# Kernel tuning notes

Measured on AMD Instinct MI355X. Metric: run time of the kernel, lower is better.

Reference implementation:

```python
import jax, jax.numpy as jnp
import numpy as np

N = 50000
E = 1000000
WIDTH = 64
DEPTH = 4


def setup_inputs() -> dict:
    key = jax.random.key(0)
    ks = jax.random.split(key, 6)
    x = jax.random.normal(ks[0], (N, 5), dtype=jnp.float32)
    edge_index = jax.random.randint(ks[1], (2, E), 0, N, dtype=jnp.int32)
    edge_attr = jax.random.normal(ks[2], (E, 3), dtype=jnp.float32)
    w1 = jax.random.normal(ks[3], (3, WIDTH), dtype=jnp.float32) / jnp.sqrt(3.0)
    b1 = jnp.zeros((WIDTH,), jnp.float32)
    w2 = jax.random.normal(ks[4], (WIDTH, 1), dtype=jnp.float32) / jnp.sqrt(float(WIDTH))
    b2 = jnp.zeros((1,), jnp.float32)
    root = jax.random.normal(ks[5], (1, 1), dtype=jnp.float32)
    bias = jnp.zeros((1,), jnp.float32)
    return dict(x=x, edge_index=edge_index, edge_attr=edge_attr,
                w1=w1, b1=b1, w2=w2, b2=b2, root=root, bias=bias)


def reference(x, edge_index, edge_attr, w1, b1, w2, b2, root, bias):
    # h: scalar node feature, column 2 of data.x -> [N, 1]
    h = x[:, 2:3]
    src, dst = edge_index[0], edge_index[1]  # messages flow src -> dst

    # Per-edge 1x1 weight from the edge MLP (depends only on edge_attr,
    # identical for all depth iterations since the conv is shared).
    w_e = jax.nn.relu(edge_attr @ w1 + b1) @ w2 + b2  # [E, 1]

    # Mean aggregation: precompute in-degree of each target node.
    deg = jax.ops.segment_sum(jnp.ones((E,), jnp.float32), dst, num_segments=N)
    inv_deg = jnp.where(deg > 0, 1.0 / jnp.maximum(deg, 1.0), 0.0)[:, None]  # [N, 1]

    for _ in range(DEPTH):
        msg = h[src] * w_e                                        # gather + per-edge weight, [E, 1]
        agg = jax.ops.segment_sum(msg, dst, num_segments=N) * inv_deg  # scatter-mean, [N, 1]
        h = jax.nn.relu(agg + h @ root + bias)                    # root transform + bias + ReLU
    return h
```

## Files before the change

### kernel.cpp

```cpp
#include <hip/hip_runtime.h>

#define NN 50000
#define NE 1000000
#define NBK 196
#define EPB 1024
#define PB 977
#define ESTRIDE 5632
#define RK 12

__global__ void init_fixed(const float* __restrict__ x, float* __restrict__ h,
                           int* __restrict__ cursor, int* __restrict__ sBeg,
                           int* __restrict__ sLim) {
    int i = blockIdx.x * 256 + threadIdx.x;
    if (i < NN) h[i] = x[5 * i + 2];
    if (i < NBK) {
        cursor[i] = i * ESTRIDE;
        sBeg[i]   = i * ESTRIDE;
        sLim[i]   = (i + 1) * ESTRIDE;
    }
}

__global__ void bucket_count(const int* __restrict__ dst, int* __restrict__ bcnt,
                             const float* __restrict__ x, float* __restrict__ h) {
    __shared__ int hist[NBK];
    int t = threadIdx.x;
    if (t < NBK) hist[t] = 0;
    __syncthreads();
    int gid = blockIdx.x * 256 + t;
    if (gid < NN) h[gid] = x[5 * gid + 2];
#pragma unroll
    for (int j = 0; j < 4; ++j) {
        int e = blockIdx.x * EPB + j * 256 + t;
        if (e < NE) atomicAdd(&hist[dst[e] >> 8], 1);
    }
    __syncthreads();
    if (t < NBK && hist[t]) atomicAdd(&bcnt[t], hist[t]);
}

__global__ void bucket_scan(const int* __restrict__ bcnt,
                            int* __restrict__ sBeg,
                            int* __restrict__ cursor,
                            int* __restrict__ sLim) {
    __shared__ int part[256];
    int t = threadIdx.x;
    int v = (t < NBK) ? ((bcnt[t] + 1) & ~1) : 0;
    part[t] = v;
    __syncthreads();
    for (int off = 1; off < 256; off <<= 1) {
        int x = part[t];
        int add = (t >= off) ? part[t - off] : 0;
        __syncthreads();
        part[t] = x + add;
        __syncthreads();
    }
    if (t < NBK) {
        int excl = part[t] - v;
        sBeg[t] = excl;
        cursor[t] = excl;
        sLim[t] = 0x7FFFFFFF;
    }
}

__global__ void place_kernel(const float* __restrict__ ea,
                             const int* __restrict__ src,
                             const int* __restrict__ dst,
                             const float* __restrict__ w1,
                             const float* __restrict__ b1,
                             const float* __restrict__ w2,
                             const float* __restrict__ b2,
                             const int* __restrict__ sLim,
                             int* __restrict__ cursor,
                             uint2* __restrict__ es,
                             int dumpbase) {
    __shared__ float sw1[192];
    __shared__ float sb1[64];
    __shared__ float sw2[64];
    __shared__ float sce[EPB];
    __shared__ int hist[NBK];
    __shared__ int hbase[NBK];
    int t = threadIdx.x;
    if (t < 192) sw1[t] = w1[t];
    if (t < 64) { sb1[t] = b1[t]; sw2[t] = w2[t]; }
    if (t < NBK) hist[t] = 0;
    __syncthreads();

    int r[4], dd[4];
#pragma unroll
    for (int j = 0; j < 4; ++j) {
        int e = blockIdx.x * EPB + j * 256 + t;
        dd[j] = -1;
        if (e < NE) {
            float a0 = ea[3 * e + 0];
            float a1 = ea[3 * e + 1];
            float a2 = ea[3 * e + 2];
            float c0 = b2[0], c1 = 0.f, c2 = 0.f, c3 = 0.f;
#pragma unroll
            for (int k = 0; k < 64; k += 4) {
                float h0 = fmaf(a0, sw1[k+0], fmaf(a1, sw1[64+k+0], fmaf(a2, sw1[128+k+0], sb1[k+0])));
                float h1 = fmaf(a0, sw1[k+1], fmaf(a1, sw1[64+k+1], fmaf(a2, sw1[128+k+1], sb1[k+1])));
                float h2 = fmaf(a0, sw1[k+2], fmaf(a1, sw1[64+k+2], fmaf(a2, sw1[128+k+2], sb1[k+2])));
                float h3 = fmaf(a0, sw1[k+3], fmaf(a1, sw1[64+k+3], fmaf(a2, sw1[128+k+3], sb1[k+3])));
                c0 = fmaf(fmaxf(h0, 0.f), sw2[k+0], c0);
                c1 = fmaf(fmaxf(h1, 0.f), sw2[k+1], c1);
                c2 = fmaf(fmaxf(h2, 0.f), sw2[k+2], c2);
                c3 = fmaf(fmaxf(h3, 0.f), sw2[k+3], c3);
            }
            sce[j * 256 + t] = (c0 + c1) + (c2 + c3);
            int d = dst[e];
            dd[j] = d;
            r[j] = atomicAdd(&hist[d >> 8], 1);
        }
    }
    __syncthreads();
    if (t < NBK) { int hv = hist[t]; if (hv) hbase[t] = atomicAdd(&cursor[t], hv); }
    __syncthreads();
#pragma unroll
    for (int j = 0; j < 4; ++j) {
        int e = blockIdx.x * EPB + j * 256 + t;
        if (e < NE) {
            int d = dd[j];
            int b = d >> 8;
            int pos = hbase[b] + r[j];
            if (pos >= sLim[b]) pos = dumpbase + (t & 63);
            unsigned pack = (unsigned)src[e] | ((unsigned)(d & 255) << 17);
            es[pos] = make_uint2(pack, __float_as_uint(sce[j * 256 + t]));
        }
    }
}

__global__ void round1_slice(const int* __restrict__ sBeg,
                             const int* __restrict__ sEnd,
                             const int* __restrict__ sLim,
                             const uint2* __restrict__ es,
                             const float* __restrict__ hold,
                             float* __restrict__ aggS,
                             int* __restrict__ degS) {
    __shared__ float lagg[256];
    __shared__ int ldeg[256];
    int t = threadIdx.x;
    int b = blockIdx.x / RK, c = blockIdx.x % RK;
    lagg[t] = 0.f;
    ldeg[t] = 0;
    __syncthreads();
    int s0 = sBeg[b];
    int s1 = sEnd[b];
    { int cap = sLim[b]; if (s1 > cap) s1 = cap; }
    const uint4* es4 = (const uint4*)es;
    for (int p = s0 + (c * 256 + t) * 2; p < s1; p += RK * 512) {
        uint4 v = es4[p >> 1];
        {
            int sidx = v.x & 0x1FFFF;
            int dl = (v.x >> 17) & 255;
            atomicAdd(&lagg[dl], hold[sidx] * __uint_as_float(v.y));
            atomicAdd(&ldeg[dl], 1);
        }
        if (p + 1 < s1) {
            int sidx = v.z & 0x1FFFF;
            int dl = (v.z >> 17) & 255;
            atomicAdd(&lagg[dl], hold[sidx] * __uint_as_float(v.w));
            atomicAdd(&ldeg[dl], 1);
        }
    }
    __syncthreads();
    int node = b * 256 + t;
    if (node < NN) {
        aggS[(size_t)c * NN + node] = lagg[t];
        degS[(size_t)c * NN + node] = ldeg[t];
    }
}

__global__ void round_slice(const int* __restrict__ sBeg,
                            const int* __restrict__ sEnd,
                            const int* __restrict__ sLim,
                            const uint2* __restrict__ es,
                            const float* __restrict__ hold,
                            float* __restrict__ aggS) {
    __shared__ float lagg[256];
    int t = threadIdx.x;
    int b = blockIdx.x / RK, c = blockIdx.x % RK;
    lagg[t] = 0.f;
    __syncthreads();
    int s0 = sBeg[b];
    int s1 = sEnd[b];
    { int cap = sLim[b]; if (s1 > cap) s1 = cap; }
    const uint4* es4 = (const uint4*)es;
    for (int p = s0 + (c * 256 + t) * 2; p < s1; p += RK * 512) {
        uint4 v = es4[p >> 1];
        {
            int sidx = v.x & 0x1FFFF;
            int dl = (v.x >> 17) & 255;
            atomicAdd(&lagg[dl], hold[sidx] * __uint_as_float(v.y));
        }
        if (p + 1 < s1) {
            int sidx = v.z & 0x1FFFF;
            int dl = (v.z >> 17) & 255;
            atomicAdd(&lagg[dl], hold[sidx] * __uint_as_float(v.w));
        }
    }
    __syncthreads();
    int node = b * 256 + t;
    if (node < NN) aggS[(size_t)c * NN + node] = lagg[t];
}

__global__ void update1(const int* __restrict__ degS,
                        const float* __restrict__ aggS,
                        float* __restrict__ invdeg,
                        const float* __restrict__ hold,
                        float* __restrict__ hnew,
                        const float* __restrict__ root,
                        const float* __restrict__ bias) {
    int i = (blockIdx.x * blockDim.x + threadIdx.x) * 2;
    if (i >= NN) return;
    float2 a = make_float2(0.f, 0.f);
    int2 d = make_int2(0, 0);
#pragma unroll
    for (int c = 0; c < RK; ++c) {
        float2 av = *(const float2*)&aggS[(size_t)c * NN + i];
        int2 dv = *(const int2*)&degS[(size_t)c * NN + i];
        a.x += av.x; a.y += av.y;
        d.x += dv.x; d.y += dv.y;
    }
    float rt = root[0], bs = bias[0];
    float2 hv = *(const float2*)&hold[i];
    float inv0 = (d.x > 0) ? (1.0f / (float)d.x) : 0.f;
    float inv1 = (d.y > 0) ? (1.0f / (float)d.y) : 0.f;
    *(float2*)&invdeg[i] = make_float2(inv0, inv1);
    float o0 = fmaxf(fmaf(hv.x, rt, fmaf(a.x, inv0, bs)), 0.f);
    float o1 = fmaxf(fmaf(hv.y, rt, fmaf(a.y, inv1, bs)), 0.f);
    *(float2*)&hnew[i] = make_float2(o0, o1);
}

__global__ void update_kernel(const float* __restrict__ aggS,
                              const float* __restrict__ invdeg,
                              const float* __restrict__ hold,
                              float* __restrict__ hnew,
                              const float* __restrict__ root,
                              const float* __restrict__ bias) {
    int i = (blockIdx.x * blockDim.x + threadIdx.x) * 2;
    if (i >= NN) return;
    float2 a = make_float2(0.f, 0.f);
#pragma unroll
    for (int c = 0; c < RK; ++c) {
        float2 av = *(const float2*)&aggS[(size_t)c * NN + i];
        a.x += av.x; a.y += av.y;
    }
    float rt = root[0], bs = bias[0];
    float2 hv = *(const float2*)&hold[i];
    float2 iv = *(const float2*)&invdeg[i];
    float o0 = fmaxf(fmaf(hv.x, rt, fmaf(a.x, iv.x, bs)), 0.f);
    float o1 = fmaxf(fmaf(hv.y, rt, fmaf(a.y, iv.y, bs)), 0.f);
    *(float2*)&hnew[i] = make_float2(o0, o1);
}


extern "C" void kernel_launch(void* const* d_in, const int* in_sizes, int n_in,
                              void* d_out, int out_size, void* d_ws, size_t ws_size,
                              hipStream_t stream) {
    const float* x    = (const float*)d_in[0];
    const int*   ei   = (const int*)d_in[1];
    const float* ea   = (const float*)d_in[2];
    const float* w1   = (const float*)d_in[3];
    const float* b1   = (const float*)d_in[4];
    const float* w2   = (const float*)d_in[5];
    const float* b2   = (const float*)d_in[6];
    const float* root = (const float*)d_in[7];
    const float* bias = (const float*)d_in[8];

    const int* src = ei;
    const int* dst = ei + NE;
    float* h = (float*)d_out;

    const int BLK = 256;
    const int gN2 = (NN / 2 + BLK - 1) / BLK;
    const int gR = NBK * RK;

    const size_t esFixed = (size_t)NBK * ESTRIDE + 64;
    const size_t needFixed = esFixed * 8
                           + (size_t)(NBK * 3) * 4
                           + (size_t)RK * NN * 4 * 2
                           + (size_t)NN * 4 * 2;

    if (ws_size >= needFixed) {
        uint2* es     = (uint2*)d_ws;
        int*   cursor = (int*)(es + esFixed);
        int*   sBeg   = cursor + NBK;
        int*   sLim   = sBeg + NBK;
        float* aggS   = (float*)(sLim + NBK);
        int*   degS   = (int*)(aggS + (size_t)RK * NN);
        float* invdeg = (float*)(degS + (size_t)RK * NN);
        float* hB     = invdeg + NN;

        init_fixed<<<NBK, BLK, 0, stream>>>(x, h, cursor, sBeg, sLim);
        place_kernel<<<PB, BLK, 0, stream>>>(ea, src, dst, w1, b1, w2, b2,
                                             sLim, cursor, es, (int)(NBK * ESTRIDE));
        round1_slice<<<gR, BLK, 0, stream>>>(sBeg, cursor, sLim, es, h, aggS, degS);
        update1<<<gN2, BLK, 0, stream>>>(degS, aggS, invdeg, h, hB, root, bias);
        round_slice<<<gR, BLK, 0, stream>>>(sBeg, cursor, sLim, es, hB, aggS);
        update_kernel<<<gN2, BLK, 0, stream>>>(aggS, invdeg, hB, h, root, bias);
        round_slice<<<gR, BLK, 0, stream>>>(sBeg, cursor, sLim, es, h, aggS);
        update_kernel<<<gN2, BLK, 0, stream>>>(aggS, invdeg, h, hB, root, bias);
        round_slice<<<gR, BLK, 0, stream>>>(sBeg, cursor, sLim, es, hB, aggS);
        update_kernel<<<gN2, BLK, 0, stream>>>(aggS, invdeg, hB, h, root, bias);
    } else {
        uint2* es     = (uint2*)d_ws;
        int*   bcnt   = (int*)(es + NE + NBK);
        int*   cursor = bcnt + NBK;
        int*   sBeg   = cursor + NBK;
        int*   sLim   = sBeg + NBK;
        float* aggS   = (float*)(sLim + NBK);
        int*   degS   = (int*)(aggS + (size_t)RK * NN);
        float* invdeg = (float*)(degS + (size_t)RK * NN);
        float* hB     = invdeg + NN;

        hipMemsetAsync(bcnt, 0, NBK * 4, stream);
        bucket_count<<<PB, BLK, 0, stream>>>(dst, bcnt, x, h);
        bucket_scan<<<1, 256, 0, stream>>>(bcnt, sBeg, cursor, sLim);
        place_kernel<<<PB, BLK, 0, stream>>>(ea, src, dst, w1, b1, w2, b2,
                                             sLim, cursor, es, 0);
        round1_slice<<<gR, BLK, 0, stream>>>(sBeg, cursor, sLim, es, h, aggS, degS);
        update1<<<gN2, BLK, 0, stream>>>(degS, aggS, invdeg, h, hB, root, bias);
        round_slice<<<gR, BLK, 0, stream>>>(sBeg, cursor, sLim, es, hB, aggS);
        update_kernel<<<gN2, BLK, 0, stream>>>(aggS, invdeg, hB, h, root, bias);
        round_slice<<<gR, BLK, 0, stream>>>(sBeg, cursor, sLim, es, h, aggS);
        update_kernel<<<gN2, BLK, 0, stream>>>(aggS, invdeg, h, hB, root, bias);
        round_slice<<<gR, BLK, 0, stream>>>(sBeg, cursor, sLim, es, hB, aggS);
        update_kernel<<<gN2, BLK, 0, stream>>>(aggS, invdeg, hB, h, root, bias);
    }
}
```

Measured before the change: 165.6 us.

## Locally sort edges by bucket in shared memory before scattering to global

Each placement block now handles 4096 edges instead of 1024. Before writing, it does a block-local counting sort by destination bucket: a shared-memory histogram, then a prefix scan, then staging of the packed edges in shared memory. The global writes to each bucket's slice therefore become contiguous runs instead of scattered 8-byte stores, and the per-bucket global cursor atomics fall by a factor of four. The cost is more shared memory, more registers from 16 unrolled edges per thread, an extra scan with many barriers, and fewer blocks (245) for occupancy.

```diff
diff --git a/kernel.cpp b/kernel.cpp
--- a/kernel.cpp
+++ b/kernel.cpp
@@ -3,8 +3,8 @@
 #define NN 50000
 #define NE 1000000
 #define NBK 196
-#define EPB 1024
-#define PB 977
+#define EPB 4096
+#define PB 245
 #define ESTRIDE 5632
 #define RK 12
 
@@ -29,7 +29,7 @@
     int gid = blockIdx.x * 256 + t;
     if (gid < NN) h[gid] = x[5 * gid + 2];
 #pragma unroll
-    for (int j = 0; j < 4; ++j) {
+    for (int j = 0; j < 16; ++j) {
         int e = blockIdx.x * EPB + j * 256 + t;
         if (e < NE) atomicAdd(&hist[dst[e] >> 8], 1);
     }
@@ -75,20 +75,26 @@
     __shared__ float sw1[192];
     __shared__ float sb1[64];
     __shared__ float sw2[64];
-    __shared__ float sce[EPB];
     __shared__ int hist[NBK];
     __shared__ int hbase[NBK];
+    __shared__ int lexcl[NBK];
+    __shared__ int part[256];
+    __shared__ unsigned spack[EPB];
+    __shared__ unsigned scev[EPB];
+    __shared__ unsigned char sbkt[EPB];
+    __shared__ int stotal;
     int t = threadIdx.x;
     if (t < 192) sw1[t] = w1[t];
     if (t < 64) { sb1[t] = b1[t]; sw2[t] = w2[t]; }
     if (t < NBK) hist[t] = 0;
     __syncthreads();
 
-    int r[4], dd[4];
-#pragma unroll
-    for (int j = 0; j < 4; ++j) {
+    unsigned pk[16], cc[16];
+    int bkrank[16];
+#pragma unroll
+    for (int j = 0; j < 16; ++j) {
         int e = blockIdx.x * EPB + j * 256 + t;
-        dd[j] = -1;
+        bkrank[j] = -1;
         if (e < NE) {
             float a0 = ea[3 * e + 0];
             float a1 = ea[3 * e + 1];
@@ -105,26 +111,46 @@
                 c2 = fmaf(fmaxf(h2, 0.f), sw2[k+2], c2);
                 c3 = fmaf(fmaxf(h3, 0.f), sw2[k+3], c3);
             }
-            sce[j * 256 + t] = (c0 + c1) + (c2 + c3);
             int d = dst[e];
-            dd[j] = d;
-            r[j] = atomicAdd(&hist[d >> 8], 1);
-        }
-    }
-    __syncthreads();
-    if (t < NBK) { int hv = hist[t]; if (hv) hbase[t] = atomicAdd(&cursor[t], hv); }
-    __syncthreads();
-#pragma unroll
-    for (int j = 0; j < 4; ++j) {
-        int e = blockIdx.x * EPB + j * 256 + t;
-        if (e < NE) {
-            int d = dd[j];
             int b = d >> 8;
-            int pos = hbase[b] + r[j];
-            if (pos >= sLim[b]) pos = dumpbase + (t & 63);
-            unsigned pack = (unsigned)src[e] | ((unsigned)(d & 255) << 17);
-            es[pos] = make_uint2(pack, __float_as_uint(sce[j * 256 + t]));
-        }
+            int rank = atomicAdd(&hist[b], 1);
+            bkrank[j] = (b << 16) | rank;
+            pk[j] = (unsigned)src[e] | ((unsigned)(d & 255) << 17);
+            cc[j] = __float_as_uint((c0 + c1) + (c2 + c3));
+        }
+    }
+    __syncthreads();
+    int hv = (t < NBK) ? hist[t] : 0;
+    if (t < NBK && hv) hbase[t] = atomicAdd(&cursor[t], hv);
+    part[t] = hv;
+    __syncthreads();
+    for (int off = 1; off < 256; off <<= 1) {
+        int xv = part[t];
+        int ad = (t >= off) ? part[t - off] : 0;
+        __syncthreads();
+        part[t] = xv + ad;
+        __syncthreads();
+    }
+    if (t < NBK) lexcl[t] = part[t] - hv;
+    if (t == 255) stotal = part[255];
+    __syncthreads();
+#pragma unroll
+    for (int j = 0; j < 16; ++j) {
+        if (bkrank[j] >= 0) {
+            int b = bkrank[j] >> 16;
+            int sl = lexcl[b] + (bkrank[j] & 0xFFFF);
+            spack[sl] = pk[j];
+            scev[sl] = cc[j];
+            sbkt[sl] = (unsigned char)b;
+        }
+    }
+    __syncthreads();
+    int tot = stotal;
+    for (int s = t; s < tot; s += 256) {
+        int b = sbkt[s];
+        int pos = hbase[b] + (s - lexcl[b]);
+        if (pos >= sLim[b]) pos = dumpbase + (t & 63);
+        es[pos] = make_uint2(spack[s], scev[s]);
     }
 }
 
```

Result: slower. 179.1 us (+8.2%).
